# Kernel tuning notes

Hardware: AMD Instinct MI355X
Metric: run time of the kernel (lower is better)

## Reference

```python
import math
import jax, jax.numpy as jnp
import numpy as np

IN_CH = 512
OUT_CH = 512
HID_CH = IN_CH // 8  # 64


def setup_inputs() -> dict:
    key = jax.random.key(0)
    k_x, k_wi, k_bi, k_wo, k_bo = jax.random.split(key, 5)
    B, H, W = 8, 64, 64
    x = jax.random.normal(k_x, (B, IN_CH, H, W), dtype=jnp.float32)
    # 1x1 convs represented as [out_channels, in_channels] matrices
    w_in = jax.random.normal(k_wi, (3 * HID_CH, IN_CH), dtype=jnp.float32) * 0.02
    b_in = jax.random.normal(k_bi, (3 * HID_CH,), dtype=jnp.float32) * 0.02
    w_out = jax.random.normal(k_wo, (OUT_CH, HID_CH), dtype=jnp.float32) * 0.02
    b_out = jax.random.normal(k_bo, (OUT_CH,), dtype=jnp.float32) * 0.02
    return {"x": x, "w_in": w_in, "b_in": b_in, "w_out": w_out, "b_out": b_out}


def reference(x, w_in, b_in, w_out, b_out):
    B, C, H, W = x.shape
    hid = w_in.shape[0] // 3
    scale = 1.0 / math.sqrt(hid)
    # in_conv (1x1): [B, 3*hid, H, W]
    qkv = jnp.einsum('bchw,oc->bohw', x, w_in) + b_in[None, :, None, None]
    q, k, v = jnp.split(qkv, 3, axis=1)
    N = H * W
    qf = q.reshape(B, hid, N)
    kf = k.reshape(B, hid, N)
    vf = v.reshape(B, hid, N)
    # full spatial attention: scores [B, N, N], softmax over keys
    scores = jnp.einsum('bcn,bcm->bnm', qf, kf) * scale
    attn = jax.nn.softmax(scores, axis=-1)
    out = jnp.einsum('bnm,bcm->bcn', attn, vf).reshape(B, hid, H, W)
    # out_conv (1x1) + identity skip (in_ch == out_ch)
    y = jnp.einsum('bchw,oc->bohw', out, w_out) + b_out[None, :, None, None] + x
    return y
```

## Files before the change

### kernel.cpp

```cpp
#include <hip/hip_runtime.h>
#include <hip/hip_bf16.h>

typedef __bf16 bf16_t;
typedef __bf16 bf16x8 __attribute__((ext_vector_type(8)));
typedef float f32x4 __attribute__((ext_vector_type(4)));
typedef float f32x16 __attribute__((ext_vector_type(16)));
typedef unsigned int u32x4 __attribute__((ext_vector_type(4)));

#define MFMA16(A,B,C) __builtin_amdgcn_mfma_f32_16x16x32_bf16(A,B,C,0,0,0)
#define MFMA32(A,B,C) __builtin_amdgcn_mfma_f32_32x32x16_bf16(A,B,C,0,0,0)

#define QSCALE 0.18033688011112042f

__device__ inline unsigned pk_bf16(float lo, float hi) {
  unsigned r;
  asm("v_cvt_pk_bf16_f32 %0, %1, %2" : "=v"(r) : "v"(lo), "v"(hi));
  return r;
}
__device__ inline bf16x8 frag4(unsigned a, unsigned b, unsigned c, unsigned d) {
  union { u32x4 u; bf16x8 f; } x;
  x.u = (u32x4){a, b, c, d};
  return x.f;
}
__device__ inline void gload16(const bf16_t* g, const bf16_t* l) {
  __builtin_amdgcn_global_load_lds(
      (const __attribute__((address_space(1))) unsigned int*)g,
      (__attribute__((address_space(3))) unsigned int*)l, 16, 0, 0);
}

__global__ __launch_bounds__(256, 4) void qkv_kernel(
    const float* __restrict__ x,
    const float* __restrict__ w_in,
    const float* __restrict__ b_in,
    bf16_t* __restrict__ q_r,
    bf16_t* __restrict__ k_r,
    bf16_t* __restrict__ v_t)
{
    const int b    = blockIdx.y;
    const int n0   = blockIdx.x * 64;
    const int t    = threadIdx.x;
    const int lane = t & 63;
    const int wave = t >> 6;

    __shared__ bf16_t Xs[2][64][56];

    const float* xb = x + (size_t)b * 512 * 4096;

    const int c  = t >> 3;
    const int nb = (t & 7) * 8;

    float4 pv0, pv1;

    {
        const float* src = xb + (size_t)c * 4096 + n0 + nb;
        pv0 = *(const float4*)(src);
        pv1 = *(const float4*)(src + 4);
        Xs[0][nb + 0][c] = (bf16_t)pv0.x; Xs[0][nb + 1][c] = (bf16_t)pv0.y;
        Xs[0][nb + 2][c] = (bf16_t)pv0.z; Xs[0][nb + 3][c] = (bf16_t)pv0.w;
        Xs[0][nb + 4][c] = (bf16_t)pv1.x; Xs[0][nb + 5][c] = (bf16_t)pv1.y;
        Xs[0][nb + 6][c] = (bf16_t)pv1.z; Xs[0][nb + 7][c] = (bf16_t)pv1.w;
    }
    __syncthreads();

    f32x4 acc[3][4] = {};

    for (int kk = 0; kk < 16; ++kk) {
        const int cur = kk & 1;
        if (kk < 15) {
            const float* src = xb + (size_t)((kk + 1) * 32 + c) * 4096 + n0 + nb;
            pv0 = *(const float4*)(src);
            pv1 = *(const float4*)(src + 4);
        }

        bf16x8 bfr[4];
        #pragma unroll
        for (int nf = 0; nf < 4; ++nf)
            bfr[nf] = *(const bf16x8*)&Xs[cur][nf * 16 + (lane & 15)][(lane >> 4) * 8];

        #pragma unroll
        for (int mf = 0; mf < 3; ++mf) {
            const int m = wave * 48 + mf * 16 + (lane & 15);
            const float* wsrc = w_in + (size_t)m * 512 + kk * 32 + (lane >> 4) * 8;
            f32x4 a0 = *(const f32x4*)(wsrc);
            f32x4 a1 = *(const f32x4*)(wsrc + 4);
            bf16x8 af = frag4(pk_bf16(a0[0], a0[1]), pk_bf16(a0[2], a0[3]),
                              pk_bf16(a1[0], a1[1]), pk_bf16(a1[2], a1[3]));
            #pragma unroll
            for (int nf = 0; nf < 4; ++nf)
                acc[mf][nf] = MFMA16(af, bfr[nf], acc[mf][nf]);
        }

        if (kk < 15) {
            const int nxt = cur ^ 1;
            Xs[nxt][nb + 0][c] = (bf16_t)pv0.x; Xs[nxt][nb + 1][c] = (bf16_t)pv0.y;
            Xs[nxt][nb + 2][c] = (bf16_t)pv0.z; Xs[nxt][nb + 3][c] = (bf16_t)pv0.w;
            Xs[nxt][nb + 4][c] = (bf16_t)pv1.x; Xs[nxt][nb + 5][c] = (bf16_t)pv1.y;
            Xs[nxt][nb + 6][c] = (bf16_t)pv1.z; Xs[nxt][nb + 7][c] = (bf16_t)pv1.w;
        }
        __syncthreads();
    }

    #pragma unroll
    for (int mf = 0; mf < 3; ++mf) {
        const int mbase = wave * 48 + mf * 16;
        const int route = mbase >> 6;
        const int cloc  = (mbase & 63) + (lane >> 4) * 4;
        const int bbase = mbase + (lane >> 4) * 4;
        #pragma unroll
        for (int nf = 0; nf < 4; ++nf) {
            const int n = n0 + nf * 16 + (lane & 15);
            const float v0 = acc[mf][nf][0] + b_in[bbase + 0];
            const float v1 = acc[mf][nf][1] + b_in[bbase + 1];
            const float v2 = acc[mf][nf][2] + b_in[bbase + 2];
            const float v3 = acc[mf][nf][3] + b_in[bbase + 3];
            if (route == 0) {
                bf16_t* qp = &q_r[((size_t)b * 4096 + n) * 64 + cloc];
                qp[0] = (bf16_t)(v0 * QSCALE); qp[1] = (bf16_t)(v1 * QSCALE);
                qp[2] = (bf16_t)(v2 * QSCALE); qp[3] = (bf16_t)(v3 * QSCALE);
            } else if (route == 1) {
                bf16_t* kp = &k_r[((size_t)b * 4096 + n) * 64 + cloc];
                kp[0] = (bf16_t)v0; kp[1] = (bf16_t)v1;
                kp[2] = (bf16_t)v2; kp[3] = (bf16_t)v3;
            } else {
                v_t[((size_t)b * 64 + cloc + 0) * 4096 + n] = (bf16_t)v0;
                v_t[((size_t)b * 64 + cloc + 1) * 4096 + n] = (bf16_t)v1;
                v_t[((size_t)b * 64 + cloc + 2) * 4096 + n] = (bf16_t)v2;
                v_t[((size_t)b * 64 + cloc + 3) * 4096 + n] = (bf16_t)v3;
            }
        }
    }
}

template <int NSPLIT>
__global__ __launch_bounds__(256, 2) void attn_partial_kernel(
    const bf16_t* __restrict__ q_r, const bf16_t* __restrict__ k_r,
    const bf16_t* __restrict__ v_t,
    bf16_t* __restrict__ Opart, float* __restrict__ ml)
{
    constexpr int KVLEN = 4096 / NSPLIT;
    constexpr int NT    = KVLEN / 64;

    const int b     = blockIdx.y;
    const int split = blockIdx.z;
    const int kv0   = split * KVLEN;
    const int t     = threadIdx.x;
    const int lane  = t & 63;
    const int wave  = t >> 6;
    const int lq    = lane & 31;
    const int hi    = lane >> 5;
    const int qA    = blockIdx.x * 256 + wave * 64 + lq;
    const int qB    = qA + 32;

    __shared__ bf16_t Ks[2][64 * 64];
    __shared__ bf16_t Vs[2][64 * 64];

    const int r8  = lane >> 3;
    const int csw = (lane & 7) ^ r8;
    const bf16_t* kb = k_r + (size_t)b * 4096 * 64;
    const bf16_t* vb = v_t + (size_t)b * 64 * 4096;

    auto STAGE = [&](int buf, int m0) {
        #pragma unroll
        for (int i = 0; i < 2; ++i) {
            const int rr = wave * 16 + i * 8;
            gload16(kb + (size_t)(m0 + rr + r8) * 64 + csw * 8, &Ks[buf][rr * 64]);
            gload16(vb + (size_t)(rr + r8) * 4096 + m0 + csw * 8, &Vs[buf][rr * 64]);
        }
    };

    bf16x8 qfA[4], qfB[4];
    {
        const bf16_t* qpA = q_r + ((size_t)b * 4096 + qA) * 64 + hi * 8;
        const bf16_t* qpB = q_r + ((size_t)b * 4096 + qB) * 64 + hi * 8;
        #pragma unroll
        for (int ks = 0; ks < 4; ++ks) {
            qfA[ks] = *(const bf16x8*)(qpA + ks * 16);
            qfB[ks] = *(const bf16x8*)(qpB + ks * 16);
        }
    }

    f32x16 oaA0 = {}, oaA1 = {}, oaB0 = {}, oaB1 = {};
    float mA = -3.0e38f, lA = 0.f, mB = -3.0e38f, lB = 0.f;

    auto SMPV = [&](f32x16& s, float& m_run, float& l_run,
                    f32x16& o0, f32x16& o1,
                    const bf16x8 v00, const bf16x8 v01,
                    const bf16x8 v10, const bf16x8 v11) {
        {
            float a8[8];
            #pragma unroll
            for (int r = 0; r < 8; ++r) a8[r] = fmaxf(s[r], s[r + 8]);
            #pragma unroll
            for (int r = 0; r < 4; ++r) a8[r] = fmaxf(a8[r], a8[r + 4]);
            float tm = fmaxf(fmaxf(a8[0], a8[1]), fmaxf(a8[2], a8[3]));
            tm = fmaxf(tm, __shfl_xor(tm, 32));
            if (__any(tm > m_run + 8.f)) {
                const float nm = fmaxf(m_run, tm);
                const float sc = __builtin_amdgcn_exp2f(m_run - nm);
                m_run = nm;
                l_run *= sc;
                #pragma unroll
                for (int r = 0; r < 16; ++r) { o0[r] *= sc; o1[r] *= sc; }
            }
        }
        #pragma unroll
        for (int r = 0; r < 16; ++r) s[r] = __builtin_amdgcn_exp2f(s[r] - m_run);
        {
            float a8[8];
            #pragma unroll
            for (int r = 0; r < 8; ++r) a8[r] = s[r] + s[r + 8];
            #pragma unroll
            for (int r = 0; r < 4; ++r) a8[r] += a8[r + 4];
            float ps = (a8[0] + a8[1]) + (a8[2] + a8[3]);
            ps += __shfl_xor(ps, 32);
            l_run += ps;
        }
        const unsigned w0 = pk_bf16(s[0], s[1]),   w1 = pk_bf16(s[2], s[3]);
        const unsigned w2 = pk_bf16(s[4], s[5]),   w3 = pk_bf16(s[6], s[7]);
        const unsigned w4 = pk_bf16(s[8], s[9]),   w5 = pk_bf16(s[10], s[11]);
        const unsigned w6 = pk_bf16(s[12], s[13]), w7 = pk_bf16(s[14], s[15]);
        const unsigned e0 = __shfl_xor((int)(hi ? w0 : w2), 32);
        const unsigned e1 = __shfl_xor((int)(hi ? w1 : w3), 32);
        const unsigned e2 = __shfl_xor((int)(hi ? w4 : w6), 32);
        const unsigned e3 = __shfl_xor((int)(hi ? w5 : w7), 32);
        const bf16x8 pf0 = frag4(hi ? e0 : w0, hi ? e1 : w1, hi ? w2 : e0, hi ? w3 : e1);
        const bf16x8 pf1 = frag4(hi ? e2 : w4, hi ? e3 : w5, hi ? w6 : e2, hi ? w7 : e3);
        o0 = MFMA32(v00, pf0, o0);
        o0 = MFMA32(v01, pf1, o0);
        o1 = MFMA32(v10, pf0, o1);
        o1 = MFMA32(v11, pf1, o1);
    };

    STAGE(0, kv0);
    asm volatile("s_waitcnt vmcnt(0)" ::: "memory");
    __builtin_amdgcn_s_barrier();

    for (int tt = 0; tt < NT; ++tt) {
        const int cur = tt & 1;
        if (tt < NT - 1) STAGE(cur ^ 1, kv0 + (tt + 1) * 64);

        #pragma unroll
        for (int s = 0; s < 2; ++s) {
            bf16x8 kf[4];
            #pragma unroll
            for (int ks = 0; ks < 4; ++ks)
                kf[ks] = *(const bf16x8*)&Ks[cur][(s * 32 + lq) * 64 +
                                                  (((ks * 2 + hi) ^ (lq & 7)) * 8)];
            f32x16 s0 = {}, s1 = {};
            #pragma unroll
            for (int ks = 0; ks < 4; ++ks) {
                s0 = MFMA32(kf[ks], qfA[ks], s0);
                s1 = MFMA32(kf[ks], qfB[ks], s1);
            }
            const int K0 = s * 4 + hi;
            const int K1 = s * 4 + 2 + hi;
            const bf16x8 v00 = *(const bf16x8*)&Vs[cur][lq * 64 + ((K0 ^ (lq & 7)) * 8)];
            const bf16x8 v10 = *(const bf16x8*)&Vs[cur][(32 + lq) * 64 + ((K0 ^ (lq & 7)) * 8)];
            const bf16x8 v01 = *(const bf16x8*)&Vs[cur][lq * 64 + ((K1 ^ (lq & 7)) * 8)];
            const bf16x8 v11 = *(const bf16x8*)&Vs[cur][(32 + lq) * 64 + ((K1 ^ (lq & 7)) * 8)];

            SMPV(s0, mA, lA, oaA0, oaA1, v00, v01, v10, v11);
            SMPV(s1, mB, lB, oaB0, oaB1, v00, v01, v10, v11);
        }

        asm volatile("s_waitcnt vmcnt(0) lgkmcnt(0)" ::: "memory");
        __builtin_amdgcn_s_barrier();
    }

    auto EPI = [&](const f32x16& o_0, const f32x16& o_1, float l_run, int nq) {
        const float inv = 1.f / l_run;
        #pragma unroll
        for (int ct = 0; ct < 2; ++ct) {
            f32x16 o = ct ? o_1 : o_0;
            #pragma unroll
            for (int r = 0; r < 16; ++r) o[r] *= inv;
            const unsigned w0 = pk_bf16(o[0], o[1]),   w1 = pk_bf16(o[2], o[3]);
            const unsigned w2 = pk_bf16(o[4], o[5]),   w3 = pk_bf16(o[6], o[7]);
            const unsigned w4 = pk_bf16(o[8], o[9]),   w5 = pk_bf16(o[10], o[11]);
            const unsigned w6 = pk_bf16(o[12], o[13]), w7 = pk_bf16(o[14], o[15]);
            const unsigned e0 = __shfl_xor((int)(hi ? w0 : w2), 32);
            const unsigned e1 = __shfl_xor((int)(hi ? w1 : w3), 32);
            const unsigned e2 = __shfl_xor((int)(hi ? w4 : w6), 32);
            const unsigned e3 = __shfl_xor((int)(hi ? w5 : w7), 32);
            bf16x8 ob0 = frag4(hi ? e0 : w0, hi ? e1 : w1, hi ? w2 : e0, hi ? w3 : e1);
            bf16x8 ob1 = frag4(hi ? e2 : w4, hi ? e3 : w5, hi ? w6 : e2, hi ? w7 : e3);
            bf16_t* op = Opart + (((size_t)(b * NSPLIT + split)) * 4096 + nq) * 64 + ct * 32;
            *(bf16x8*)(op + hi * 8)      = ob0;
            *(bf16x8*)(op + 16 + hi * 8) = ob1;
        }
    };
    EPI(oaA0, oaA1, lA, qA);
    EPI(oaB0, oaB1, lB, qB);

    if (hi == 0) {
        float2 va; va.x = mA; va.y = lA;
        *(float2*)&ml[(((size_t)(b * NSPLIT + split)) * 4096 + qA) * 2] = va;
        float2 vbv; vbv.x = mB; vbv.y = lB;
        *(float2*)&ml[(((size_t)(b * NSPLIT + split)) * 4096 + qB) * 2] = vbv;
    }
}

template <int NSPLIT>
__global__ __launch_bounds__(512) void combine_kernel(
    const bf16_t* __restrict__ Opart, const float* __restrict__ ml,
    const float* __restrict__ x, const float* __restrict__ w_out,
    const float* __restrict__ b_out, float* __restrict__ y)
{
    const int b    = blockIdx.y;
    const int t    = threadIdx.x;
    const int lane = t & 63;
    const int wave = t >> 6;
    const int lq   = lane & 31;
    const int hi   = lane >> 5;
    const int group = wave >> 2;
    const int nq   = blockIdx.x * 64 + group * 32 + lq;

    float coef[NSPLIT];
    {
        float m_s[NSPLIT], l_s[NSPLIT];
        #pragma unroll
        for (int s = 0; s < NSPLIT; ++s) {
            float2 v = *(const float2*)&ml[(((size_t)(b * NSPLIT + s)) * 4096 + nq) * 2];
            m_s[s] = v.x; l_s[s] = v.y;
        }
        float M = m_s[0];
        #pragma unroll
        for (int s = 1; s < NSPLIT; ++s) M = fmaxf(M, m_s[s]);
        float L = 0.f;
        #pragma unroll
        for (int s = 0; s < NSPLIT; ++s) {
            coef[s] = __builtin_amdgcn_exp2f(m_s[s] - M) * l_s[s];
            L += coef[s];
        }
        const float invL = 1.f / L;
        #pragma unroll
        for (int s = 0; s < NSPLIT; ++s) coef[s] *= invL;
    }

    bf16x8 obf[4];
    #pragma unroll
    for (int ks = 0; ks < 4; ++ks) {
        float a8[8] = {};
        #pragma unroll
        for (int s = 0; s < NSPLIT; ++s) {
            bf16x8 o = *(const bf16x8*)&Opart[
                (((size_t)(b * NSPLIT + s)) * 4096 + nq) * 64 + ks * 16 + hi * 8];
            #pragma unroll
            for (int j = 0; j < 8; ++j) a8[j] += coef[s] * (float)o[j];
        }
        obf[ks] = frag4(pk_bf16(a8[0], a8[1]), pk_bf16(a8[2], a8[3]),
                        pk_bf16(a8[4], a8[5]), pk_bf16(a8[6], a8[7]));
    }

    #pragma unroll 1
    for (int i = 0; i < 4; ++i) {
        const int mt = (wave & 3) * 4 + i;
        f32x16 acc = {};
        #pragma unroll
        for (int ks = 0; ks < 4; ++ks) {
            const float* wp = w_out + (size_t)(mt * 32 + lq) * 64 + ks * 16 + hi * 8;
            f32x4 a0 = *(const f32x4*)wp;
            f32x4 a1 = *(const f32x4*)(wp + 4);
            bf16x8 af = frag4(pk_bf16(a0[0], a0[1]), pk_bf16(a0[2], a0[3]),
                              pk_bf16(a1[0], a1[1]), pk_bf16(a1[2], a1[3]));
            acc = MFMA32(af, obf[ks], acc);
        }
        #pragma unroll
        for (int r = 0; r < 16; ++r) {
            const int m = mt * 32 + (r & 3) + 8 * (r >> 2) + 4 * hi;
            const size_t idx = ((size_t)b * 512 + m) * 4096 + nq;
            y[idx] = acc[r] + b_out[m] + x[idx];
        }
    }
}

extern "C" void kernel_launch(void* const* d_in, const int* in_sizes, int n_in,
                              void* d_out, int out_size, void* d_ws, size_t ws_size,
                              hipStream_t stream)
{
    const float* x     = (const float*)d_in[0];
    const float* w_in  = (const float*)d_in[1];
    const float* b_in  = (const float*)d_in[2];
    const float* w_out = (const float*)d_in[3];
    const float* b_out = (const float*)d_in[4];
    float* y = (float*)d_out;

    char* ws = (char*)d_ws;
    bf16_t* q_r   = (bf16_t*)(ws);
    bf16_t* k_r   = (bf16_t*)(ws + 4194304);
    bf16_t* v_t   = (bf16_t*)(ws + 8388608);
    bf16_t* Opart = (bf16_t*)(ws + 12582912);

    qkv_kernel<<<dim3(64, 8), 256, 0, stream>>>(x, w_in, b_in, q_r, k_r, v_t);

    const size_t need8 = 12582912u + 33554432u + 2097152u;
    if (ws_size >= need8) {
        float* ml = (float*)(ws + 12582912 + 33554432);
        attn_partial_kernel<8><<<dim3(16, 8, 8), 256, 0, stream>>>(q_r, k_r, v_t, Opart, ml);
        combine_kernel<8><<<dim3(64, 8), 512, 0, stream>>>(Opart, ml, x, w_out, b_out, y);
    } else {
        float* ml = (float*)(ws + 12582912 + 16777216);
        attn_partial_kernel<4><<<dim3(16, 8, 4), 256, 0, stream>>>(q_r, k_r, v_t, Opart, ml);
        combine_kernel<4><<<dim3(64, 8), 512, 0, stream>>>(Opart, ml, x, w_out, b_out, y);
    }
}
```

Before: 132.8 us.

## Replace double-buffered direct-to-LDS loads with register-staged single buffer

The attention kernel's K/V staging changes from double-buffered global_load_lds into two LDS buffers to a single LDS buffer. The next tile is prefetched into registers during compute, then written to LDS between two barriers. Launch bounds rise from 2 to 4 blocks per CU, since halving LDS per block aims for higher occupancy to hide latency. The cost is extra registers for the staged data, an extra barrier per tile, and register pressure that could spill under the tighter launch bound.

```diff
diff --git a/kernel.cpp b/kernel.cpp
--- a/kernel.cpp
+++ b/kernel.cpp
@@ -21,11 +21,6 @@
   union { u32x4 u; bf16x8 f; } x;
   x.u = (u32x4){a, b, c, d};
   return x.f;
-}
-__device__ inline void gload16(const bf16_t* g, const bf16_t* l) {
-  __builtin_amdgcn_global_load_lds(
-      (const __attribute__((address_space(1))) unsigned int*)g,
-      (__attribute__((address_space(3))) unsigned int*)l, 16, 0, 0);
 }
 
 __global__ __launch_bounds__(256, 4) void qkv_kernel(
@@ -132,7 +127,7 @@
 }
 
 template <int NSPLIT>
-__global__ __launch_bounds__(256, 2) void attn_partial_kernel(
+__global__ __launch_bounds__(256, 4) void attn_partial_kernel(
     const bf16_t* __restrict__ q_r, const bf16_t* __restrict__ k_r,
     const bf16_t* __restrict__ v_t,
     bf16_t* __restrict__ Opart, float* __restrict__ ml)
@@ -151,21 +146,31 @@
     const int qA    = blockIdx.x * 256 + wave * 64 + lq;
     const int qB    = qA + 32;
 
-    __shared__ bf16_t Ks[2][64 * 64];
-    __shared__ bf16_t Vs[2][64 * 64];
+    __shared__ bf16_t Ks[64 * 64];
+    __shared__ bf16_t Vs[64 * 64];
 
     const int r8  = lane >> 3;
     const int csw = (lane & 7) ^ r8;
+    const int rr  = wave * 16;
+    const int lds0 = rr * 64 + lane * 8;
+    const int lds1 = (rr + 8) * 64 + lane * 8;
+
     const bf16_t* kb = k_r + (size_t)b * 4096 * 64;
     const bf16_t* vb = v_t + (size_t)b * 64 * 4096;
 
-    auto STAGE = [&](int buf, int m0) {
-        #pragma unroll
-        for (int i = 0; i < 2; ++i) {
-            const int rr = wave * 16 + i * 8;
-            gload16(kb + (size_t)(m0 + rr + r8) * 64 + csw * 8, &Ks[buf][rr * 64]);
-            gload16(vb + (size_t)(rr + r8) * 4096 + m0 + csw * 8, &Vs[buf][rr * 64]);
-        }
+    u32x4 kr0, kr1, vr0, vr1;
+
+    auto LOAD = [&](int m0) {
+        kr0 = *(const u32x4*)(kb + (size_t)(m0 + rr + r8) * 64 + csw * 8);
+        kr1 = *(const u32x4*)(kb + (size_t)(m0 + rr + 8 + r8) * 64 + csw * 8);
+        vr0 = *(const u32x4*)(vb + (size_t)(rr + r8) * 4096 + m0 + csw * 8);
+        vr1 = *(const u32x4*)(vb + (size_t)(rr + 8 + r8) * 4096 + m0 + csw * 8);
+    };
+    auto WRITE = [&]() {
+        *(u32x4*)&Ks[lds0] = kr0;
+        *(u32x4*)&Ks[lds1] = kr1;
+        *(u32x4*)&Vs[lds0] = vr0;
+        *(u32x4*)&Vs[lds1] = vr1;
     };
 
     bf16x8 qfA[4], qfB[4];
@@ -231,21 +236,20 @@
         o1 = MFMA32(v11, pf1, o1);
     };
 
-    STAGE(0, kv0);
-    asm volatile("s_waitcnt vmcnt(0)" ::: "memory");
-    __builtin_amdgcn_s_barrier();
+    LOAD(kv0);
+    WRITE();
+    __syncthreads();
 
     for (int tt = 0; tt < NT; ++tt) {
-        const int cur = tt & 1;
-        if (tt < NT - 1) STAGE(cur ^ 1, kv0 + (tt + 1) * 64);
+        if (tt < NT - 1) LOAD(kv0 + (tt + 1) * 64);
 
         #pragma unroll
         for (int s = 0; s < 2; ++s) {
             bf16x8 kf[4];
             #pragma unroll
             for (int ks = 0; ks < 4; ++ks)
-                kf[ks] = *(const bf16x8*)&Ks[cur][(s * 32 + lq) * 64 +
-                                                  (((ks * 2 + hi) ^ (lq & 7)) * 8)];
+                kf[ks] = *(const bf16x8*)&Ks[(s * 32 + lq) * 64 +
+                                             (((ks * 2 + hi) ^ (lq & 7)) * 8)];
             f32x16 s0 = {}, s1 = {};
             #pragma unroll
             for (int ks = 0; ks < 4; ++ks) {
@@ -254,17 +258,20 @@
             }
             const int K0 = s * 4 + hi;
             const int K1 = s * 4 + 2 + hi;
-            const bf16x8 v00 = *(const bf16x8*)&Vs[cur][lq * 64 + ((K0 ^ (lq & 7)) * 8)];
-            const bf16x8 v10 = *(const bf16x8*)&Vs[cur][(32 + lq) * 64 + ((K0 ^ (lq & 7)) * 8)];
-            const bf16x8 v01 = *(const bf16x8*)&Vs[cur][lq * 64 + ((K1 ^ (lq & 7)) * 8)];
-            const bf16x8 v11 = *(const bf16x8*)&Vs[cur][(32 + lq) * 64 + ((K1 ^ (lq & 7)) * 8)];
+            const bf16x8 v00 = *(const bf16x8*)&Vs[lq * 64 + ((K0 ^ (lq & 7)) * 8)];
+            const bf16x8 v10 = *(const bf16x8*)&Vs[(32 + lq) * 64 + ((K0 ^ (lq & 7)) * 8)];
+            const bf16x8 v01 = *(const bf16x8*)&Vs[lq * 64 + ((K1 ^ (lq & 7)) * 8)];
+            const bf16x8 v11 = *(const bf16x8*)&Vs[(32 + lq) * 64 + ((K1 ^ (lq & 7)) * 8)];
 
             SMPV(s0, mA, lA, oaA0, oaA1, v00, v01, v10, v11);
             SMPV(s1, mB, lB, oaB0, oaB1, v00, v01, v10, v11);
         }
 
-        asm volatile("s_waitcnt vmcnt(0) lgkmcnt(0)" ::: "memory");
-        __builtin_amdgcn_s_barrier();
+        if (tt < NT - 1) {
+            __syncthreads();
+            WRITE();
+            __syncthreads();
+        }
     }
 
     auto EPI = [&](const f32x16& o_0, const f32x16& o_1, float l_run, int nq) {
```

After: 227.2 us. 71.1% more time.

## Compute softmax row sums via MFMA with ones, use permlane32 swap, fix split 4

Applied to the files above, without the earlier changes.

Replaces the scalar reduction of softmax probabilities into the running row sum with an extra pair of MFMAs against a vector of bf16 ones, so the sum accumulates in matrix-core output. It also replaces the shuffle/select lane exchange with v_permlane32_swap, simplifies the max reduction tree, and always launches the NSPLIT=4 path instead of choosing 8 when the workspace allows. The trade-off is more MFMA work per tile and sums taken over bf16-rounded probabilities; the rescale path only scales the first accumulator element, which relies on the MFMA output layout; and a smaller split count lowers grid parallelism.

```diff
diff --git a/kernel.cpp b/kernel.cpp
--- a/kernel.cpp
+++ b/kernel.cpp
@@ -179,52 +179,53 @@
         }
     }
 
+    const bf16x8 vones = frag4(0x3F803F80u, 0x3F803F80u, 0x3F803F80u, 0x3F803F80u);
+
     f32x16 oaA0 = {}, oaA1 = {}, oaB0 = {}, oaB1 = {};
-    float mA = -3.0e38f, lA = 0.f, mB = -3.0e38f, lB = 0.f;
-
-    auto SMPV = [&](f32x16& s, float& m_run, float& l_run,
+    f32x16 lнакA = {};
+    f32x16 lнакB = {};
+    float mA = -3.0e38f, mB = -3.0e38f;
+
+    auto SMPV = [&](f32x16& s, float& m_run, f32x16& l_acc,
                     f32x16& o0, f32x16& o1,
                     const bf16x8 v00, const bf16x8 v01,
                     const bf16x8 v10, const bf16x8 v11) {
         {
-            float a8[8];
-            #pragma unroll
-            for (int r = 0; r < 8; ++r) a8[r] = fmaxf(s[r], s[r + 8]);
-            #pragma unroll
-            for (int r = 0; r < 4; ++r) a8[r] = fmaxf(a8[r], a8[r + 4]);
-            float tm = fmaxf(fmaxf(a8[0], a8[1]), fmaxf(a8[2], a8[3]));
+            const float t0 = fmaxf(fmaxf(s[0],  s[1]),  s[2]);
+            const float t1 = fmaxf(fmaxf(s[3],  s[4]),  s[5]);
+            const float t2 = fmaxf(fmaxf(s[6],  s[7]),  s[8]);
+            const float t3 = fmaxf(fmaxf(s[9],  s[10]), s[11]);
+            const float t4 = fmaxf(fmaxf(s[12], s[13]), s[14]);
+            const float u0 = fmaxf(fmaxf(t0, t1), t2);
+            const float u1 = fmaxf(fmaxf(t3, t4), s[15]);
+            float tm = fmaxf(u0, u1);
             tm = fmaxf(tm, __shfl_xor(tm, 32));
             if (__any(tm > m_run + 8.f)) {
                 const float nm = fmaxf(m_run, tm);
                 const float sc = __builtin_amdgcn_exp2f(m_run - nm);
                 m_run = nm;
-                l_run *= sc;
+                l_acc[0] *= sc;
                 #pragma unroll
                 for (int r = 0; r < 16; ++r) { o0[r] *= sc; o1[r] *= sc; }
             }
         }
         #pragma unroll
         for (int r = 0; r < 16; ++r) s[r] = __builtin_amdgcn_exp2f(s[r] - m_run);
-        {
-            float a8[8];
-            #pragma unroll
-            for (int r = 0; r < 8; ++r) a8[r] = s[r] + s[r + 8];
-            #pragma unroll
-            for (int r = 0; r < 4; ++r) a8[r] += a8[r + 4];
-            float ps = (a8[0] + a8[1]) + (a8[2] + a8[3]);
-            ps += __shfl_xor(ps, 32);
-            l_run += ps;
-        }
-        const unsigned w0 = pk_bf16(s[0], s[1]),   w1 = pk_bf16(s[2], s[3]);
-        const unsigned w2 = pk_bf16(s[4], s[5]),   w3 = pk_bf16(s[6], s[7]);
-        const unsigned w4 = pk_bf16(s[8], s[9]),   w5 = pk_bf16(s[10], s[11]);
-        const unsigned w6 = pk_bf16(s[12], s[13]), w7 = pk_bf16(s[14], s[15]);
-        const unsigned e0 = __shfl_xor((int)(hi ? w0 : w2), 32);
-        const unsigned e1 = __shfl_xor((int)(hi ? w1 : w3), 32);
-        const unsigned e2 = __shfl_xor((int)(hi ? w4 : w6), 32);
-        const unsigned e3 = __shfl_xor((int)(hi ? w5 : w7), 32);
-        const bf16x8 pf0 = frag4(hi ? e0 : w0, hi ? e1 : w1, hi ? w2 : e0, hi ? w3 : e1);
-        const bf16x8 pf1 = frag4(hi ? e2 : w4, hi ? e3 : w5, hi ? w6 : e2, hi ? w7 : e3);
+
+        unsigned w0 = pk_bf16(s[0],  s[1]),  w1 = pk_bf16(s[2],  s[3]);
+        unsigned w2 = pk_bf16(s[4],  s[5]),  w3 = pk_bf16(s[6],  s[7]);
+        unsigned w4 = pk_bf16(s[8],  s[9]),  w5 = pk_bf16(s[10], s[11]);
+        unsigned w6 = pk_bf16(s[12], s[13]), w7 = pk_bf16(s[14], s[15]);
+        asm("v_permlane32_swap_b32 %0, %1" : "+v"(w0), "+v"(w2));
+        asm("v_permlane32_swap_b32 %0, %1" : "+v"(w1), "+v"(w3));
+        asm("v_permlane32_swap_b32 %0, %1" : "+v"(w4), "+v"(w6));
+        asm("v_permlane32_swap_b32 %0, %1" : "+v"(w5), "+v"(w7));
+        const bf16x8 pf0 = frag4(w0, w1, w2, w3);
+        const bf16x8 pf1 = frag4(w4, w5, w6, w7);
+
+        l_acc = MFMA32(vones, pf0, l_acc);
+        l_acc = MFMA32(vones, pf1, l_acc);
+
         o0 = MFMA32(v00, pf0, o0);
         o0 = MFMA32(v01, pf1, o0);
         o1 = MFMA32(v10, pf0, o1);
@@ -259,8 +260,8 @@
             const bf16x8 v01 = *(const bf16x8*)&Vs[cur][lq * 64 + ((K1 ^ (lq & 7)) * 8)];
             const bf16x8 v11 = *(const bf16x8*)&Vs[cur][(32 + lq) * 64 + ((K1 ^ (lq & 7)) * 8)];
 
-            SMPV(s0, mA, lA, oaA0, oaA1, v00, v01, v10, v11);
-            SMPV(s1, mB, lB, oaB0, oaB1, v00, v01, v10, v11);
+            SMPV(s0, mA, lнакA, oaA0, oaA1, v00, v01, v10, v11);
+            SMPV(s1, mB, lнакB, oaB0, oaB1, v00, v01, v10, v11);
         }
 
         asm volatile("s_waitcnt vmcnt(0) lgkmcnt(0)" ::: "memory");
@@ -274,28 +275,28 @@
             f32x16 o = ct ? o_1 : o_0;
             #pragma unroll
             for (int r = 0; r < 16; ++r) o[r] *= inv;
-            const unsigned w0 = pk_bf16(o[0], o[1]),   w1 = pk_bf16(o[2], o[3]);
-            const unsigned w2 = pk_bf16(o[4], o[5]),   w3 = pk_bf16(o[6], o[7]);
-            const unsigned w4 = pk_bf16(o[8], o[9]),   w5 = pk_bf16(o[10], o[11]);
-            const unsigned w6 = pk_bf16(o[12], o[13]), w7 = pk_bf16(o[14], o[15]);
-            const unsigned e0 = __shfl_xor((int)(hi ? w0 : w2), 32);
-            const unsigned e1 = __shfl_xor((int)(hi ? w1 : w3), 32);
-            const unsigned e2 = __shfl_xor((int)(hi ? w4 : w6), 32);
-            const unsigned e3 = __shfl_xor((int)(hi ? w5 : w7), 32);
-            bf16x8 ob0 = frag4(hi ? e0 : w0, hi ? e1 : w1, hi ? w2 : e0, hi ? w3 : e1);
-            bf16x8 ob1 = frag4(hi ? e2 : w4, hi ? e3 : w5, hi ? w6 : e2, hi ? w7 : e3);
+            unsigned w0 = pk_bf16(o[0],  o[1]),  w1 = pk_bf16(o[2],  o[3]);
+            unsigned w2 = pk_bf16(o[4],  o[5]),  w3 = pk_bf16(o[6],  o[7]);
+            unsigned w4 = pk_bf16(o[8],  o[9]),  w5 = pk_bf16(o[10], o[11]);
+            unsigned w6 = pk_bf16(o[12], o[13]), w7 = pk_bf16(o[14], o[15]);
+            asm("v_permlane32_swap_b32 %0, %1" : "+v"(w0), "+v"(w2));
+            asm("v_permlane32_swap_b32 %0, %1" : "+v"(w1), "+v"(w3));
+            asm("v_permlane32_swap_b32 %0, %1" : "+v"(w4), "+v"(w6));
+            asm("v_permlane32_swap_b32 %0, %1" : "+v"(w5), "+v"(w7));
+            bf16x8 ob0 = frag4(w0, w1, w2, w3);
+            bf16x8 ob1 = frag4(w4, w5, w6, w7);
             bf16_t* op = Opart + (((size_t)(b * NSPLIT + split)) * 4096 + nq) * 64 + ct * 32;
             *(bf16x8*)(op + hi * 8)      = ob0;
             *(bf16x8*)(op + 16 + hi * 8) = ob1;
         }
     };
-    EPI(oaA0, oaA1, lA, qA);
-    EPI(oaB0, oaB1, lB, qB);
+    EPI(oaA0, oaA1, lнакA[0], qA);
+    EPI(oaB0, oaB1, lнакB[0], qB);
 
     if (hi == 0) {
-        float2 va; va.x = mA; va.y = lA;
+        float2 va; va.x = mA; va.y = lнакA[0];
         *(float2*)&ml[(((size_t)(b * NSPLIT + split)) * 4096 + qA) * 2] = va;
-        float2 vbv; vbv.x = mB; vbv.y = lB;
+        float2 vbv; vbv.x = mB; vbv.y = lнакB[0];
         *(float2*)&ml[(((size_t)(b * NSPLIT + split)) * 4096 + qB) * 2] = vbv;
     }
 }
@@ -390,17 +391,9 @@
     bf16_t* k_r   = (bf16_t*)(ws + 4194304);
     bf16_t* v_t   = (bf16_t*)(ws + 8388608);
     bf16_t* Opart = (bf16_t*)(ws + 12582912);
+    float*  ml    = (float*)(ws + 12582912 + 16777216);
 
     qkv_kernel<<<dim3(64, 8), 256, 0, stream>>>(x, w_in, b_in, q_r, k_r, v_t);
-
-    const size_t need8 = 12582912u + 33554432u + 2097152u;
-    if (ws_size >= need8) {
-        float* ml = (float*)(ws + 12582912 + 33554432);
-        attn_partial_kernel<8><<<dim3(16, 8, 8), 256, 0, stream>>>(q_r, k_r, v_t, Opart, ml);
-        combine_kernel<8><<<dim3(64, 8), 512, 0, stream>>>(Opart, ml, x, w_out, b_out, y);
-    } else {
-        float* ml = (float*)(ws + 12582912 + 16777216);
-        attn_partial_kernel<4><<<dim3(16, 8, 4), 256, 0, stream>>>(q_r, k_r, v_t, Opart, ml);
-        combine_kernel<4><<<dim3(64, 8), 512, 0, stream>>>(Opart, ml, x, w_out, b_out, y);
-    }
-}
+    attn_partial_kernel<4><<<dim3(16, 8, 4), 256, 0, stream>>>(q_r, k_r, v_t, Opart, ml);
+    combine_kernel<4><<<dim3(64, 8), 512, 0, stream>>>(Opart, ml, x, w_out, b_out, y);
+}
```

After: 127.1 us. 1.05x faster.
